# Performance work log

Measured on AMD Instinct MI355X. Metric: run time of the kernel, lower is better.

The kernel has to match this reference:

```python
import jax, jax.numpy as jnp
import numpy as np
from jax import lax

B, T, MEL, D, H, NC = 8, 256, 128, 192, 4, 20
C_EVENT, C_SCENE = 8, 64
ETA, LR, ALPHA = 0.9, 0.1, 0.01  # memory momentum, write lr, forget rate
EPS = 1e-5


def _ln(x, g, b):
    m = x.mean(-1, keepdims=True)
    v = ((x - m) ** 2).mean(-1, keepdims=True)
    return (x - m) / jnp.sqrt(v + EPS) * g + b


def _mem_step(x, t, M, S, Wk, Wv, Wq, chunk):
    # x: [B,D]; M,S: [B,D,D]. Titans-style neural memory, updated every `chunk` steps.
    k = x @ Wk
    v = x @ Wv
    q = x @ Wq
    err = v - jnp.einsum('bd,bde->be', k, M)          # surprise / prediction error
    S_new = ETA * S + LR * jnp.einsum('bd,be->bde', k, err)
    M_new = (1.0 - ALPHA) * M + S_new
    upd = (t % chunk) == 0
    S = jnp.where(upd, S_new, S)
    M = jnp.where(upd, M_new, M)
    out = jnp.einsum('bd,bde->be', q, M)              # retrieval
    return out, M, S


def setup_inputs() -> dict:
    key = jax.random.key(0)
    ks = jax.random.split(key, 24)
    w = lambda k, shp, s=0.05: jax.random.normal(k, shp, dtype=jnp.float32) * s
    inp = {
        'x': jax.random.normal(ks[0], (B, T, MEL), dtype=jnp.float32),
        'W_in': w(ks[1], (MEL, D)), 'b_in': jnp.zeros((D,), jnp.float32),
        # MHA at seq_len=1: softmax over one key -> weight 1, so only V and out proj matter
        'Wv_a': w(ks[2], (D, D)), 'bv_a': jnp.zeros((D,), jnp.float32),
        'Wo_a': w(ks[3], (D, D)), 'bo_a': jnp.zeros((D,), jnp.float32),
        # conformer conv module (degenerate seq_len=1: depthwise conv -> center tap)
        'ln1_g': jnp.ones((D,), jnp.float32), 'ln1_b': jnp.zeros((D,), jnp.float32),
        'pw1_w': w(ks[4], (D, 2 * D)), 'pw1_b': jnp.zeros((2 * D,), jnp.float32),
        'dw_w': w(ks[5], (D,), 0.2), 'dw_b': jnp.zeros((D,), jnp.float32),
        'bn_s': jnp.ones((D,), jnp.float32), 'bn_b': jnp.zeros((D,), jnp.float32),
        'pw2_w': w(ks[6], (D, D)), 'pw2_b': jnp.zeros((D,), jnp.float32),
        # theta (event) / delta (scene) neural memory projections
        'Wk_t': w(ks[7], (D, D)), 'Wv_t': w(ks[8], (D, D)), 'Wq_t': w(ks[9], (D, D)),
        'Wk_d': w(ks[10], (D, D)), 'Wv_d': w(ks[11], (D, D)), 'Wq_d': w(ks[12], (D, D)),
        'ln2_g': jnp.ones((D,), jnp.float32), 'ln2_b': jnp.zeros((D,), jnp.float32),
        'Wc': w(ks[13], (D, NC)), 'bc': jnp.zeros((NC,), jnp.float32),
    }
    return inp


def reference(x, W_in, b_in, Wv_a, bv_a, Wo_a, bo_a, ln1_g, ln1_b, pw1_w, pw1_b,
              dw_w, dw_b, bn_s, bn_b, pw2_w, pw2_b, Wk_t, Wv_t, Wq_t,
              Wk_d, Wv_d, Wq_d, ln2_g, ln2_b, Wc, bc):
    xp = x @ W_in + b_in                               # [B,T,D]

    def step(carry, inp):
        x_t, t = inp                                   # x_t: [B,D]
        Mt, St, Md, Sd = carry
        d_out, Md, Sd = _mem_step(x_t, t, Md, Sd, Wk_d, Wv_d, Wq_d, C_SCENE)
        x1 = x_t + 0.5 * d_out
        attn = (x1 @ Wv_a + bv_a) @ Wo_a + bo_a        # single-token self-attn
        x2 = x1 + attn
        h = _ln(x2, ln1_g, ln1_b)
        h = h @ pw1_w + pw1_b
        a, g = jnp.split(h, 2, axis=-1)
        h = a * jax.nn.sigmoid(g)                      # GLU
        h = h * dw_w + dw_b                            # depthwise conv center tap
        h = h * bn_s + bn_b                            # eval-mode BN
        h = jax.nn.silu(h)
        h = h @ pw2_w + pw2_b
        x3 = x2 + h
        t_out, Mt, St = _mem_step(x3, t, Mt, St, Wk_t, Wv_t, Wq_t, C_EVENT)
        x4 = x3 + 0.5 * t_out
        return (Mt, St, Md, Sd), _ln(x4, ln2_g, ln2_b)

    z = jnp.zeros((B, D, D), jnp.float32)
    xs = (jnp.swapaxes(xp, 0, 1), jnp.arange(T))       # [T,B,D], [T]
    _, ys = lax.scan(step, (z, z, z, z), xs)
    y = jnp.swapaxes(ys, 0, 1)                         # [B,T,D]
    pooled = y.mean(axis=1)
    return pooled @ Wc + bc                            # [B,NC]
```

## Files before the change

kernel.cpp:

```cpp
#include <hip/hip_runtime.h>
#include <math.h>

#define Bb 8
#define Tt 256
#define MEL 128
#define Dd 192
#define NCc 20
#define ND 4
#define NT 32
#define ETAc 0.9f
#define LRc 0.1f
#define MDEC 0.99f
#define EPSc 1e-5f
#define PT 4
#define PTILES 64
#define RTT 8
#define PADD 196

__device__ __forceinline__ float sigmoidf_(float x) {
    return 1.0f / (1.0f + __expf(-x));
}

__device__ __forceinline__ float memcoef(int n, int i) {
    float m = LRc, pw = LRc;
    for (int nn = i + 1; nn <= n; nn++) { pw *= ETAc; m = MDEC * m + pw; }
    return m;
}

__device__ __forceinline__ float dot4(float4 a, float4 b) {
    return a.x * b.x + a.y * b.y + a.z * b.z + a.w * b.w;
}

__global__ __launch_bounds__(192) void prep(
    const float* __restrict__ Wv_a, const float* __restrict__ Wo_a,
    const float* __restrict__ bv_a, const float* __restrict__ bo_a,
    const float* __restrict__ Wq_t, const float* __restrict__ Wq_d,
    const float* __restrict__ x, const float* __restrict__ W_in,
    const float* __restrict__ b_in, const float* __restrict__ Wk_d,
    const float* __restrict__ Wv_d,
    float* __restrict__ Wavo_ws, float* __restrict__ b_avo,
    float* __restrict__ WqtT, float* __restrict__ WqdT,
    float* __restrict__ Kd_ws, float* __restrict__ Vd_ws,
    float* __restrict__ pooled)
{
    __shared__ __align__(16) float smem[512];
    int blk = blockIdx.x, tid = threadIdx.x;

    if (blk < 192) {
        int m = blk;
        smem[tid] = Wv_a[m * Dd + tid];
        __syncthreads();
        int o = tid;
        float acc = 0.f;
        #pragma unroll 8
        for (int k = 0; k < Dd; k += 4) {
            acc += Wo_a[(k + 0) * Dd + o] * smem[k + 0];
            acc += Wo_a[(k + 1) * Dd + o] * smem[k + 1];
            acc += Wo_a[(k + 2) * Dd + o] * smem[k + 2];
            acc += Wo_a[(k + 3) * Dd + o] * smem[k + 3];
        }
        Wavo_ws[m * Dd + o] = acc;
        return;
    }
    if (blk == 192) {
        int o = tid;
        float s = bo_a[o];
        #pragma unroll 4
        for (int m = 0; m < Dd; m++) s += bv_a[m] * Wo_a[m * Dd + o];
        b_avo[o] = s;
        return;
    }
    if (blk < 241) {
        int r0 = 4 * (blk - 193);
        float4 v;
        v.x = Wq_t[(r0 + 0) * Dd + tid];
        v.y = Wq_t[(r0 + 1) * Dd + tid];
        v.z = Wq_t[(r0 + 2) * Dd + tid];
        v.w = Wq_t[(r0 + 3) * Dd + tid];
        *(float4*)&WqtT[tid * Dd + r0] = v;
        return;
    }
    if (blk < 289) {
        int r0 = 4 * (blk - 241);
        float4 v;
        v.x = Wq_d[(r0 + 0) * Dd + tid];
        v.y = Wq_d[(r0 + 1) * Dd + tid];
        v.z = Wq_d[(r0 + 2) * Dd + tid];
        v.w = Wq_d[(r0 + 3) * Dd + tid];
        *(float4*)&WqdT[tid * Dd + r0] = v;
        return;
    }
    if (blk == 321) {
        for (int q = tid; q < Bb * Dd; q += 192) pooled[q] = 0.f;
        return;
    }

    int q = blk - 289;
    int b = q >> 2, i = q & 3;
    float* XR = smem;
    float* XP = smem + 128;
    if (tid < 128) XR[tid] = x[((size_t)b * Tt + 64 * i) * MEL + tid];
    __syncthreads();
    {
        int o = tid;
        float acc = b_in[o];
        #pragma unroll 8
        for (int k = 0; k < MEL; k += 4) {
            acc += W_in[(k + 0) * Dd + o] * XR[k + 0];
            acc += W_in[(k + 1) * Dd + o] * XR[k + 1];
            acc += W_in[(k + 2) * Dd + o] * XR[k + 2];
            acc += W_in[(k + 3) * Dd + o] * XR[k + 3];
        }
        XP[o] = acc;
    }
    __syncthreads();
    {
        int o = tid;
        float ak = 0.f, av = 0.f;
        #pragma unroll 4
        for (int k = 0; k < Dd; k += 4) {
            float x0 = XP[k + 0], x1 = XP[k + 1], x2 = XP[k + 2], x3 = XP[k + 3];
            ak += Wk_d[(k + 0) * Dd + o] * x0 + Wk_d[(k + 1) * Dd + o] * x1
                + Wk_d[(k + 2) * Dd + o] * x2 + Wk_d[(k + 3) * Dd + o] * x3;
            av += Wv_d[(k + 0) * Dd + o] * x0 + Wv_d[(k + 1) * Dd + o] * x1
                + Wv_d[(k + 2) * Dd + o] * x2 + Wv_d[(k + 3) * Dd + o] * x3;
        }
        Kd_ws[(b * ND + i) * Dd + o] = ak;
        Vd_ws[(b * ND + i) * Dd + o] = av;
    }
}

__global__ __launch_bounds__(192) void delta_solve(
    const float* __restrict__ WqdT, const float* __restrict__ Kd_ws,
    float* __restrict__ Vd_ws, float* __restrict__ Ud_ws)
{
    int blk = blockIdx.x, b = blk / 5, role = blk % 5, tid = threadIdx.x;
    if (role == 0) {
        __shared__ __align__(16) float K4[ND][Dd], V4[ND][Dd];
        __shared__ float G[16], mc[16];
        for (int q = tid; q < ND * 48; q += 192) {
            int i = q / 48, c = q - i * 48;
            ((float4*)K4[i])[c] = ((const float4*)&Kd_ws[(b * ND + i) * Dd])[c];
            ((float4*)V4[i])[c] = ((const float4*)&Vd_ws[(b * ND + i) * Dd])[c];
        }
        __syncthreads();
        if (tid < 16) {
            int i = tid >> 2, j = tid & 3;
            float s = 0.f;
            for (int d = 0; d < Dd; d++) s += K4[i][d] * K4[j][d];
            G[tid] = s;
            mc[tid] = (j <= i) ? memcoef(i, j) : 0.f;
        }
        __syncthreads();
        for (int i = 1; i < ND; i++) {
            float acc = V4[i][tid];
            for (int m = 0; m < i; m++)
                acc -= mc[(i - 1) * ND + m] * G[i * ND + m] * V4[m][tid];
            V4[i][tid] = acc;
            __syncthreads();
        }
        for (int i = 0; i < ND; i++) Vd_ws[(b * ND + i) * Dd + tid] = V4[i][tid];
    } else {
        __shared__ float KS[Dd];
        int i = role - 1;
        KS[tid] = Kd_ws[(b * ND + i) * Dd + tid];
        __syncthreads();
        int o = tid;
        float acc = 0.f;
        #pragma unroll 8
        for (int k = 0; k < Dd; k += 4) {
            acc += WqdT[(k + 0) * Dd + o] * KS[k + 0];
            acc += WqdT[(k + 1) * Dd + o] * KS[k + 1];
            acc += WqdT[(k + 2) * Dd + o] * KS[k + 2];
            acc += WqdT[(k + 3) * Dd + o] * KS[k + 3];
        }
        Ud_ws[(b * ND + i) * Dd + o] = acc;
    }
}

__global__ __launch_bounds__(192) void pipeline(
    const float* __restrict__ x, const float* __restrict__ W_in,
    const float* __restrict__ b_in,
    const float* __restrict__ ln1_g, const float* __restrict__ ln1_b,
    const float* __restrict__ pw1_w, const float* __restrict__ pw1_b,
    const float* __restrict__ dw_w, const float* __restrict__ dw_b,
    const float* __restrict__ bn_s, const float* __restrict__ bn_b,
    const float* __restrict__ pw2_w, const float* __restrict__ pw2_b,
    const float* __restrict__ Wavo_ws, const float* __restrict__ b_avo,
    const float* __restrict__ Ed_ws, const float* __restrict__ Ud_ws,
    float* __restrict__ x3_ws)
{
    int blk = blockIdx.x;
    int b = blk >> 6, tile = blk & 63;
    int t0 = tile * PT, n = tile >> 4;
    int tid = threadIdx.x;

    __shared__ __align__(16) float XR[PT][MEL];
    __shared__ __align__(16) float XP[PT][Dd];
    __shared__ __align__(16) float ED[ND][PADD], UD[ND][PADD];
    __shared__ __align__(16) float X1[PT][Dd], X2[PT][Dd];
    __shared__ __align__(16) float LNX[PT][Dd], HG[PT][Dd];
    __shared__ float WQs[PT * ND];
    __shared__ float mv[PT][2];

    if (tid < 128) {
        int r = tid >> 5, c = tid & 31;
        ((float4*)XR[r])[c] = ((const float4*)&x[((size_t)b * Tt + t0 + r) * MEL])[c];
    }
    for (int q = tid; q < ND * 48 * 2; q += 192) {
        int which = q >= ND * 48;
        int qq = which ? q - ND * 48 : q;
        int i = qq / 48, c = qq - i * 48;
        if (!which) ((float4*)ED[i])[c] = ((const float4*)&Ed_ws[(b * ND + i) * Dd])[c];
        else        ((float4*)UD[i])[c] = ((const float4*)&Ud_ws[(b * ND + i) * Dd])[c];
    }
    __syncthreads();

    int o = tid;
    {
        float acc[PT];
        float bb = b_in[o];
        #pragma unroll
        for (int r = 0; r < PT; r++) acc[r] = bb;
        #pragma unroll 8
        for (int k = 0; k < MEL; k += 4) {
            float w0 = W_in[(k + 0) * Dd + o], w1 = W_in[(k + 1) * Dd + o];
            float w2 = W_in[(k + 2) * Dd + o], w3 = W_in[(k + 3) * Dd + o];
            #pragma unroll
            for (int r = 0; r < PT; r++) {
                float4 xv = *(const float4*)&XR[r][k];
                acc[r] += w0 * xv.x + w1 * xv.y + w2 * xv.z + w3 * xv.w;
            }
        }
        #pragma unroll
        for (int r = 0; r < PT; r++) XP[r][tid] = acc[r];
    }
    __syncthreads();

    if (tid < 128) {
        int r = tid >> 5, i = (tid >> 3) & 3, c = tid & 7;
        float s = 0.f;
        const float* xp = XP[r];
        const float* u = UD[i];
        #pragma unroll
        for (int j = 0; j < 24; j++) s += xp[c * 24 + j] * u[c * 24 + j];
        s += __shfl_down(s, 4, 8);
        s += __shfl_down(s, 2, 8);
        s += __shfl_down(s, 1, 8);
        if (c == 0) {
            float coef = (i <= n) ? memcoef(n, i) : 0.f;
            WQs[r * ND + i] = s * coef;
        }
    }
    __syncthreads();

    {
        #pragma unroll
        for (int r = 0; r < PT; r++) {
            float dout = WQs[r * ND + 0] * ED[0][tid] + WQs[r * ND + 1] * ED[1][tid]
                       + WQs[r * ND + 2] * ED[2][tid] + WQs[r * ND + 3] * ED[3][tid];
            X1[r][tid] = XP[r][tid] + 0.5f * dout;
        }
    }
    __syncthreads();

    {
        float acc[PT];
        float bb = b_avo[o];
        #pragma unroll
        for (int r = 0; r < PT; r++) acc[r] = bb;
        #pragma unroll 8
        for (int k = 0; k < Dd; k += 4) {
            float w0 = Wavo_ws[(k + 0) * Dd + o], w1 = Wavo_ws[(k + 1) * Dd + o];
            float w2 = Wavo_ws[(k + 2) * Dd + o], w3 = Wavo_ws[(k + 3) * Dd + o];
            #pragma unroll
            for (int r = 0; r < PT; r++) {
                float4 xv = *(const float4*)&X1[r][k];
                acc[r] += w0 * xv.x + w1 * xv.y + w2 * xv.z + w3 * xv.w;
            }
        }
        #pragma unroll
        for (int r = 0; r < PT; r++) X2[r][tid] = X1[r][tid] + acc[r];
    }
    __syncthreads();

    if (tid < 128) {
        int r = tid >> 5, j = tid & 31;
        float s = 0.f, sq = 0.f;
        for (int d = j; d < Dd; d += 32) { float v = X2[r][d]; s += v; sq += v * v; }
        for (int off = 16; off > 0; off >>= 1) {
            s += __shfl_down(s, off, 32); sq += __shfl_down(sq, off, 32);
        }
        if (j == 0) {
            float mean = s / Dd;
            mv[r][0] = mean;
            mv[r][1] = rsqrtf(sq / Dd - mean * mean + EPSc);
        }
    }
    __syncthreads();
    {
        float g = ln1_g[tid], bb = ln1_b[tid];
        #pragma unroll
        for (int r = 0; r < PT; r++)
            LNX[r][tid] = (X2[r][tid] - mv[r][0]) * mv[r][1] * g + bb;
    }
    __syncthreads();

    {
        float aa[PT], gg[PT];
        float ba = pw1_b[o], bg = pw1_b[o + Dd];
        #pragma unroll
        for (int r = 0; r < PT; r++) { aa[r] = ba; gg[r] = bg; }
        #pragma unroll 4
        for (int k = 0; k < Dd; k += 4) {
            float wa0 = pw1_w[(k + 0) * 2 * Dd + o], wg0 = pw1_w[(k + 0) * 2 * Dd + Dd + o];
            float wa1 = pw1_w[(k + 1) * 2 * Dd + o], wg1 = pw1_w[(k + 1) * 2 * Dd + Dd + o];
            float wa2 = pw1_w[(k + 2) * 2 * Dd + o], wg2 = pw1_w[(k + 2) * 2 * Dd + Dd + o];
            float wa3 = pw1_w[(k + 3) * 2 * Dd + o], wg3 = pw1_w[(k + 3) * 2 * Dd + Dd + o];
            #pragma unroll
            for (int r = 0; r < PT; r++) {
                float4 xv = *(const float4*)&LNX[r][k];
                aa[r] += wa0 * xv.x + wa1 * xv.y + wa2 * xv.z + wa3 * xv.w;
                gg[r] += wg0 * xv.x + wg1 * xv.y + wg2 * xv.z + wg3 * xv.w;
            }
        }
        float dww = dw_w[o], dwb = dw_b[o], bns = bn_s[o], bnb = bn_b[o];
        #pragma unroll
        for (int r = 0; r < PT; r++) {
            float h = aa[r] * sigmoidf_(gg[r]);
            h = h * dww + dwb;
            h = h * bns + bnb;
            h = h * sigmoidf_(h);
            HG[r][tid] = h;
        }
    }
    __syncthreads();

    {
        float acc[PT];
        float bb = pw2_b[o];
        #pragma unroll
        for (int r = 0; r < PT; r++) acc[r] = bb;
        #pragma unroll 8
        for (int k = 0; k < Dd; k += 4) {
            float w0 = pw2_w[(k + 0) * Dd + o], w1 = pw2_w[(k + 1) * Dd + o];
            float w2 = pw2_w[(k + 2) * Dd + o], w3 = pw2_w[(k + 3) * Dd + o];
            #pragma unroll
            for (int r = 0; r < PT; r++) {
                float4 xv = *(const float4*)&HG[r][k];
                acc[r] += w0 * xv.x + w1 * xv.y + w2 * xv.z + w3 * xv.w;
            }
        }
        #pragma unroll
        for (int r = 0; r < PT; r++)
            x3_ws[((size_t)b * Tt + t0 + r) * Dd + tid] = X2[r][tid] + acc[r];
    }
}

__global__ __launch_bounds__(192) void theta_projU(
    const float* __restrict__ x3_ws,
    const float* __restrict__ Wk_t, const float* __restrict__ Wv_t,
    const float* __restrict__ WqtT,
    float* __restrict__ Kt_ws, float* __restrict__ Vt_ws,
    float* __restrict__ Ut_ws)
{
    int blk = blockIdx.x, b = blk >> 5, i = blk & 31;
    int tid = threadIdx.x;
    __shared__ float XS[Dd];
    __shared__ float KS[Dd];

    XS[tid] = x3_ws[((size_t)b * Tt + 8 * i) * Dd + tid];
    __syncthreads();

    int o = tid;
    float ak = 0.f, av = 0.f;
    #pragma unroll 4
    for (int k = 0; k < Dd; k += 4) {
        float x0 = XS[k + 0], x1 = XS[k + 1], x2 = XS[k + 2], x3 = XS[k + 3];
        ak += Wk_t[(k + 0) * Dd + o] * x0 + Wk_t[(k + 1) * Dd + o] * x1
            + Wk_t[(k + 2) * Dd + o] * x2 + Wk_t[(k + 3) * Dd + o] * x3;
        av += Wv_t[(k + 0) * Dd + o] * x0 + Wv_t[(k + 1) * Dd + o] * x1
            + Wv_t[(k + 2) * Dd + o] * x2 + Wv_t[(k + 3) * Dd + o] * x3;
    }
    Kt_ws[(b * NT + i) * Dd + o] = ak;
    Vt_ws[(b * NT + i) * Dd + o] = av;
    KS[o] = ak;
    __syncthreads();

    float au = 0.f;
    #pragma unroll 8
    for (int k = 0; k < Dd; k += 4) {
        au += WqtT[(k + 0) * Dd + o] * KS[k + 0];
        au += WqtT[(k + 1) * Dd + o] * KS[k + 1];
        au += WqtT[(k + 2) * Dd + o] * KS[k + 2];
        au += WqtT[(k + 3) * Dd + o] * KS[k + 3];
    }
    Ut_ws[(b * NT + i) * Dd + o] = au;
}

__global__ __launch_bounds__(192) void theta_solve(
    const float* __restrict__ Kt_ws, float* __restrict__ Vt_ws)
{
    int b = blockIdx.x, tid = threadIdx.x;
    __shared__ __align__(16) float K[NT][PADD], E[NT][PADD];
    __shared__ float G[NT * NT], mc[NT * NT];

    for (int q = tid; q < NT * 48; q += 192) {
        int i = q / 48, c = q - i * 48;
        ((float4*)K[i])[c] = ((const float4*)&Kt_ws[(b * NT + i) * Dd])[c];
        ((float4*)E[i])[c] = ((const float4*)&Vt_ws[(b * NT + i) * Dd])[c];
    }
    if (tid < NT) {
        int i = tid;
        float m = 0.f, pw = LRc;
        for (int nn = 0; nn < NT; nn++) {
            float v;
            if (nn < i) v = 0.f;
            else if (nn == i) { m = LRc; v = m; }
            else { pw *= ETAc; m = MDEC * m + pw; v = m; }
            mc[nn * NT + i] = v;
        }
    }
    __syncthreads();
    for (int p = tid; p < NT * NT; p += 192) {
        int i = p >> 5, j = p & 31;
        const float4* ki = (const float4*)K[i];
        const float4* kj = (const float4*)K[j];
        float s = 0.f;
        #pragma unroll 4
        for (int kk = 0; kk < 48; kk++) s += dot4(ki[kk], kj[kk]);
        G[p] = s;
    }
    __syncthreads();
    for (int i = 1; i < NT; i++) {
        float acc = E[i][tid];
        #pragma unroll 4
        for (int m = 0; m < i; m++)
            acc -= mc[(i - 1) * NT + m] * G[i * NT + m] * E[m][tid];
        E[i][tid] = acc;
        __syncthreads();
    }
    for (int i = 0; i < NT; i++) Vt_ws[(b * NT + i) * Dd + tid] = E[i][tid];
}

__global__ __launch_bounds__(256) void retrieve(
    const float* __restrict__ x3_ws, const float* __restrict__ Ut_ws,
    const float* __restrict__ Et_ws, const float* __restrict__ ln2_g,
    const float* __restrict__ ln2_b, float* __restrict__ pooled)
{
    int blk = blockIdx.x, b = blk >> 5, tile = blk & 31;
    int t0 = tile * RTT, n = tile;
    int tid = threadIdx.x;

    __shared__ __align__(16) float UT[NT][PADD];
    __shared__ __align__(16) float XS[RTT][PADD];
    __shared__ float WQ[RTT * NT];
    __shared__ float mv[RTT][2];

    for (int q = tid; q < NT * 48; q += 256) {
        int i = q / 48, c = q - i * 48;
        ((float4*)UT[i])[c] = ((const float4*)&Ut_ws[(b * NT + i) * Dd])[c];
    }
    for (int q = tid; q < RTT * 48; q += 256) {
        int r = q / 48, c = q - r * 48;
        ((float4*)XS[r])[c] = ((const float4*)&x3_ws[((size_t)b * Tt + t0 + r) * Dd])[c];
    }
    __syncthreads();

    {
        int r = tid >> 5, i = tid & 31;
        const float4* u4 = (const float4*)UT[i];
        const float4* x4 = (const float4*)XS[r];
        float s = 0.f;
        #pragma unroll 8
        for (int kk = 0; kk < 48; kk++) s += dot4(u4[kk], x4[kk]);
        float coef = (i <= n) ? memcoef(n, i) : 0.f;
        WQ[tid] = s * coef;
    }
    __syncthreads();

    if (tid < Dd) {
        float acc[RTT] = {};
        #pragma unroll 4
        for (int i = 0; i < NT; i++) {
            float e = Et_ws[(b * NT + i) * Dd + tid];
            #pragma unroll
            for (int r = 0; r < RTT; r++) acc[r] += WQ[r * NT + i] * e;
        }
        #pragma unroll
        for (int r = 0; r < RTT; r++) XS[r][tid] += 0.5f * acc[r];
    }
    __syncthreads();

    {
        int r = tid >> 5, j = tid & 31;
        float s = 0.f, sq = 0.f;
        for (int d = j; d < Dd; d += 32) { float v = XS[r][d]; s += v; sq += v * v; }
        for (int off = 16; off > 0; off >>= 1) {
            s += __shfl_down(s, off, 32); sq += __shfl_down(sq, off, 32);
        }
        if (j == 0) {
            float mean = s / Dd;
            mv[r][0] = mean;
            mv[r][1] = rsqrtf(sq / Dd - mean * mean + EPSc);
        }
    }
    __syncthreads();

    if (tid < Dd) {
        float g = ln2_g[tid], bb = ln2_b[tid];
        float sum = 0.f;
        #pragma unroll
        for (int r = 0; r < RTT; r++)
            sum += (XS[r][tid] - mv[r][0]) * mv[r][1] * g + bb;
        atomicAdd(&pooled[b * Dd + tid], sum);
    }
}

__global__ __launch_bounds__(192) void head(
    const float* __restrict__ pooled, const float* __restrict__ Wc,
    const float* __restrict__ bc, float* __restrict__ out)
{
    int tid = threadIdx.x;
    if (tid < Bb * NCc) {
        int b = tid / NCc, c = tid - b * NCc;
        float s = 0.f;
        for (int d = 0; d < Dd; d++) s += pooled[b * Dd + d] * Wc[d * NCc + c];
        out[tid] = s * (1.0f / Tt) + bc[c];
    }
}

extern "C" void kernel_launch(void* const* d_in, const int* in_sizes, int n_in,
                              void* d_out, int out_size, void* d_ws, size_t ws_size,
                              hipStream_t stream) {
    const float* x     = (const float*)d_in[0];
    const float* W_in  = (const float*)d_in[1];
    const float* b_in  = (const float*)d_in[2];
    const float* Wv_a  = (const float*)d_in[3];
    const float* bv_a  = (const float*)d_in[4];
    const float* Wo_a  = (const float*)d_in[5];
    const float* bo_a  = (const float*)d_in[6];
    const float* ln1_g = (const float*)d_in[7];
    const float* ln1_b = (const float*)d_in[8];
    const float* pw1_w = (const float*)d_in[9];
    const float* pw1_b = (const float*)d_in[10];
    const float* dw_w  = (const float*)d_in[11];
    const float* dw_b  = (const float*)d_in[12];
    const float* bn_s  = (const float*)d_in[13];
    const float* bn_b  = (const float*)d_in[14];
    const float* pw2_w = (const float*)d_in[15];
    const float* pw2_b = (const float*)d_in[16];
    const float* Wk_t  = (const float*)d_in[17];
    const float* Wv_t  = (const float*)d_in[18];
    const float* Wq_t  = (const float*)d_in[19];
    const float* Wk_d  = (const float*)d_in[20];
    const float* Wv_d  = (const float*)d_in[21];
    const float* Wq_d  = (const float*)d_in[22];
    const float* ln2_g = (const float*)d_in[23];
    const float* ln2_b = (const float*)d_in[24];
    const float* Wc    = (const float*)d_in[25];
    const float* bc    = (const float*)d_in[26];

    float* ws = (float*)d_ws;
    size_t off = 0;
    float* x3_ws   = ws + off; off += (size_t)Bb * Tt * Dd;
    float* Kd_ws   = ws + off; off += Bb * ND * Dd;
    float* Vd_ws   = ws + off; off += Bb * ND * Dd;
    float* Ud_ws   = ws + off; off += Bb * ND * Dd;
    float* Kt_ws   = ws + off; off += Bb * NT * Dd;
    float* Vt_ws   = ws + off; off += Bb * NT * Dd;
    float* Ut_ws   = ws + off; off += Bb * NT * Dd;
    float* pooled  = ws + off; off += Bb * Dd;
    float* Wavo_ws = ws + off; off += Dd * Dd;
    float* WqtT    = ws + off; off += Dd * Dd;
    float* WqdT    = ws + off; off += Dd * Dd;
    float* b_avo   = ws + off; off += Dd;

    prep<<<322, 192, 0, stream>>>(
        Wv_a, Wo_a, bv_a, bo_a, Wq_t, Wq_d,
        x, W_in, b_in, Wk_d, Wv_d,
        Wavo_ws, b_avo, WqtT, WqdT, Kd_ws, Vd_ws, pooled);
    delta_solve<<<Bb * 5, 192, 0, stream>>>(WqdT, Kd_ws, Vd_ws, Ud_ws);
    pipeline<<<Bb * PTILES, 192, 0, stream>>>(
        x, W_in, b_in, ln1_g, ln1_b, pw1_w, pw1_b, dw_w, dw_b,
        bn_s, bn_b, pw2_w, pw2_b, Wavo_ws, b_avo, Vd_ws, Ud_ws, x3_ws);
    theta_projU<<<Bb * NT, 192, 0, stream>>>(
        x3_ws, Wk_t, Wv_t, WqtT, Kt_ws, Vt_ws, Ut_ws);
    theta_solve<<<Bb, 192, 0, stream>>>(Kt_ws, Vt_ws);
    retrieve<<<Bb * 32, 256, 0, stream>>>(
        x3_ws, Ut_ws, Vt_ws, ln2_g, ln2_b, pooled);
    head<<<1, 192, 0, stream>>>(pooled, Wc, bc, (float*)d_out);
}
```

Before: 207.2 us.

## Halve pipeline/retrieve tiles, batch Wavo rows, register-resident triangular theta solve

The pipeline and retrieve kernels now use half-size time tiles, doubling the number of blocks to spread work over more compute units. In prep, each Wavo block computes four output rows at once, so fewer blocks reread Wo_a. The theta_solve kernel folds the memory coefficients into a strictly lower-triangular matrix, computing only the needed Gram entries. It then runs forward substitution in registers with no per-step __syncthreads. Retrieve splits each dot product across two lanes with a shuffle; the cost is more redundant loads of the shared U/E data per block and fewer rows per block.

```diff
diff --git a/kernel.cpp b/kernel.cpp
--- a/kernel.cpp
+++ b/kernel.cpp
@@ -12,9 +12,9 @@
 #define LRc 0.1f
 #define MDEC 0.99f
 #define EPSc 1e-5f
-#define PT 4
-#define PTILES 64
-#define RTT 8
+#define PT 2
+#define PTILES 128
+#define RTT 4
 #define PADD 196
 
 __device__ __forceinline__ float sigmoidf_(float x) {
@@ -43,26 +43,30 @@
     float* __restrict__ Kd_ws, float* __restrict__ Vd_ws,
     float* __restrict__ pooled)
 {
-    __shared__ __align__(16) float smem[512];
+    __shared__ __align__(16) float smem[768];
     int blk = blockIdx.x, tid = threadIdx.x;
 
-    if (blk < 192) {
-        int m = blk;
-        smem[tid] = Wv_a[m * Dd + tid];
+    if (blk < 48) {
+        int m0 = blk * 4;
+        for (int q = tid; q < 4 * Dd; q += 192) smem[q] = Wv_a[m0 * Dd + q];
         __syncthreads();
         int o = tid;
-        float acc = 0.f;
-        #pragma unroll 8
-        for (int k = 0; k < Dd; k += 4) {
-            acc += Wo_a[(k + 0) * Dd + o] * smem[k + 0];
-            acc += Wo_a[(k + 1) * Dd + o] * smem[k + 1];
-            acc += Wo_a[(k + 2) * Dd + o] * smem[k + 2];
-            acc += Wo_a[(k + 3) * Dd + o] * smem[k + 3];
-        }
-        Wavo_ws[m * Dd + o] = acc;
+        float a0 = 0.f, a1 = 0.f, a2 = 0.f, a3 = 0.f;
+        #pragma unroll 4
+        for (int k = 0; k < Dd; k += 2) {
+            float w0 = Wo_a[(k + 0) * Dd + o], w1 = Wo_a[(k + 1) * Dd + o];
+            a0 += w0 * smem[0 * Dd + k] + w1 * smem[0 * Dd + k + 1];
+            a1 += w0 * smem[1 * Dd + k] + w1 * smem[1 * Dd + k + 1];
+            a2 += w0 * smem[2 * Dd + k] + w1 * smem[2 * Dd + k + 1];
+            a3 += w0 * smem[3 * Dd + k] + w1 * smem[3 * Dd + k + 1];
+        }
+        Wavo_ws[(m0 + 0) * Dd + o] = a0;
+        Wavo_ws[(m0 + 1) * Dd + o] = a1;
+        Wavo_ws[(m0 + 2) * Dd + o] = a2;
+        Wavo_ws[(m0 + 3) * Dd + o] = a3;
         return;
     }
-    if (blk == 192) {
+    if (blk == 48) {
         int o = tid;
         float s = bo_a[o];
         #pragma unroll 4
@@ -70,8 +74,8 @@
         b_avo[o] = s;
         return;
     }
-    if (blk < 241) {
-        int r0 = 4 * (blk - 193);
+    if (blk < 97) {
+        int r0 = 4 * (blk - 49);
         float4 v;
         v.x = Wq_t[(r0 + 0) * Dd + tid];
         v.y = Wq_t[(r0 + 1) * Dd + tid];
@@ -80,8 +84,8 @@
         *(float4*)&WqtT[tid * Dd + r0] = v;
         return;
     }
-    if (blk < 289) {
-        int r0 = 4 * (blk - 241);
+    if (blk < 145) {
+        int r0 = 4 * (blk - 97);
         float4 v;
         v.x = Wq_d[(r0 + 0) * Dd + tid];
         v.y = Wq_d[(r0 + 1) * Dd + tid];
@@ -90,12 +94,12 @@
         *(float4*)&WqdT[tid * Dd + r0] = v;
         return;
     }
-    if (blk == 321) {
+    if (blk == 177) {
         for (int q = tid; q < Bb * Dd; q += 192) pooled[q] = 0.f;
         return;
     }
 
-    int q = blk - 289;
+    int q = blk - 145;
     int b = q >> 2, i = q & 3;
     float* XR = smem;
     float* XP = smem + 128;
@@ -191,8 +195,8 @@
     float* __restrict__ x3_ws)
 {
     int blk = blockIdx.x;
-    int b = blk >> 6, tile = blk & 63;
-    int t0 = tile * PT, n = tile >> 4;
+    int b = blk >> 7, tile = blk & 127;
+    int t0 = tile * PT, n = tile >> 5;
     int tid = threadIdx.x;
 
     __shared__ __align__(16) float XR[PT][MEL];
@@ -203,7 +207,7 @@
     __shared__ float WQs[PT * ND];
     __shared__ float mv[PT][2];
 
-    if (tid < 128) {
+    if (tid < PT * 32) {
         int r = tid >> 5, c = tid & 31;
         ((float4*)XR[r])[c] = ((const float4*)&x[((size_t)b * Tt + t0 + r) * MEL])[c];
     }
@@ -237,7 +241,7 @@
     }
     __syncthreads();
 
-    if (tid < 128) {
+    if (tid < PT * 32) {
         int r = tid >> 5, i = (tid >> 3) & 3, c = tid & 7;
         float s = 0.f;
         const float* xp = XP[r];
@@ -284,7 +288,7 @@
     }
     __syncthreads();
 
-    if (tid < 128) {
+    if (tid < PT * 32) {
         int r = tid >> 5, j = tid & 31;
         float s = 0.f, sq = 0.f;
         for (int d = j; d < Dd; d += 32) { float v = X2[r][d]; s += v; sq += v * v; }
@@ -402,13 +406,12 @@
     const float* __restrict__ Kt_ws, float* __restrict__ Vt_ws)
 {
     int b = blockIdx.x, tid = threadIdx.x;
-    __shared__ __align__(16) float K[NT][PADD], E[NT][PADD];
-    __shared__ float G[NT * NT], mc[NT * NT];
+    __shared__ __align__(16) float K[NT][PADD];
+    __shared__ float A[NT * NT], mc[NT * NT];
 
     for (int q = tid; q < NT * 48; q += 192) {
         int i = q / 48, c = q - i * 48;
         ((float4*)K[i])[c] = ((const float4*)&Kt_ws[(b * NT + i) * Dd])[c];
-        ((float4*)E[i])[c] = ((const float4*)&Vt_ws[(b * NT + i) * Dd])[c];
     }
     if (tid < NT) {
         int i = tid;
@@ -424,23 +427,30 @@
     __syncthreads();
     for (int p = tid; p < NT * NT; p += 192) {
         int i = p >> 5, j = p & 31;
-        const float4* ki = (const float4*)K[i];
-        const float4* kj = (const float4*)K[j];
         float s = 0.f;
-        #pragma unroll 4
-        for (int kk = 0; kk < 48; kk++) s += dot4(ki[kk], kj[kk]);
-        G[p] = s;
-    }
-    __syncthreads();
+        if (j < i) {
+            const float4* ki = (const float4*)K[i];
+            const float4* kj = (const float4*)K[j];
+            float g = 0.f;
+            #pragma unroll 4
+            for (int kk = 0; kk < 48; kk++) g += dot4(ki[kk], kj[kk]);
+            s = mc[(i - 1) * NT + j] * g;
+        }
+        A[p] = s;
+    }
+    __syncthreads();
+    float e[NT];
+    #pragma unroll
+    for (int i = 0; i < NT; i++) e[i] = Vt_ws[(b * NT + i) * Dd + tid];
+    #pragma unroll
     for (int i = 1; i < NT; i++) {
-        float acc = E[i][tid];
-        #pragma unroll 4
-        for (int m = 0; m < i; m++)
-            acc -= mc[(i - 1) * NT + m] * G[i * NT + m] * E[m][tid];
-        E[i][tid] = acc;
-        __syncthreads();
-    }
-    for (int i = 0; i < NT; i++) Vt_ws[(b * NT + i) * Dd + tid] = E[i][tid];
+        float acc = e[i];
+        #pragma unroll
+        for (int m = 0; m < i; m++) acc -= A[i * NT + m] * e[m];
+        e[i] = acc;
+    }
+    #pragma unroll
+    for (int i = 0; i < NT; i++) Vt_ws[(b * NT + i) * Dd + tid] = e[i];
 }
 
 __global__ __launch_bounds__(256) void retrieve(
@@ -448,8 +458,8 @@
     const float* __restrict__ Et_ws, const float* __restrict__ ln2_g,
     const float* __restrict__ ln2_b, float* __restrict__ pooled)
 {
-    int blk = blockIdx.x, b = blk >> 5, tile = blk & 31;
-    int t0 = tile * RTT, n = tile;
+    int blk = blockIdx.x, b = blk >> 6, tile = blk & 63;
+    int t0 = tile * RTT, n = tile >> 1;
     int tid = threadIdx.x;
 
     __shared__ __align__(16) float UT[NT][PADD];
@@ -468,14 +478,17 @@
     __syncthreads();
 
     {
-        int r = tid >> 5, i = tid & 31;
+        int r = tid >> 6, i = (tid >> 1) & 31, h = tid & 1;
         const float4* u4 = (const float4*)UT[i];
         const float4* x4 = (const float4*)XS[r];
         float s = 0.f;
         #pragma unroll 8
-        for (int kk = 0; kk < 48; kk++) s += dot4(u4[kk], x4[kk]);
-        float coef = (i <= n) ? memcoef(n, i) : 0.f;
-        WQ[tid] = s * coef;
+        for (int kk = h * 24; kk < h * 24 + 24; kk++) s += dot4(u4[kk], x4[kk]);
+        s += __shfl_down(s, 1, 2);
+        if (h == 0) {
+            float coef = (i <= n) ? memcoef(n, i) : 0.f;
+            WQ[r * NT + i] = s * coef;
+        }
     }
     __syncthreads();
 
@@ -492,7 +505,7 @@
     }
     __syncthreads();
 
-    {
+    if (tid < RTT * 32) {
         int r = tid >> 5, j = tid & 31;
         float s = 0.f, sq = 0.f;
         for (int d = j; d < Dd; d += 32) { float v = XS[r][d]; s += v; sq += v * v; }
@@ -576,7 +589,7 @@
     float* WqdT    = ws + off; off += Dd * Dd;
     float* b_avo   = ws + off; off += Dd;
 
-    prep<<<322, 192, 0, stream>>>(
+    prep<<<178, 192, 0, stream>>>(
         Wv_a, Wo_a, bv_a, bo_a, Wq_t, Wq_d,
         x, W_in, b_in, Wk_d, Wv_d,
         Wavo_ws, b_avo, WqtT, WqdT, Kd_ws, Vd_ws, pooled);
@@ -587,7 +600,7 @@
     theta_projU<<<Bb * NT, 192, 0, stream>>>(
         x3_ws, Wk_t, Wv_t, WqtT, Kt_ws, Vt_ws, Ut_ws);
     theta_solve<<<Bb, 192, 0, stream>>>(Kt_ws, Vt_ws);
-    retrieve<<<Bb * 32, 256, 0, stream>>>(
+    retrieve<<<Bb * 64, 256, 0, stream>>>(
         x3_ws, Ut_ws, Vt_ws, ln2_g, ln2_b, pooled);
     head<<<1, 192, 0, stream>>>(pooled, Wc, bc, (float*)d_out);
 }
```

New measurement: 195.2 us, median of 2. 1.06x faster.
